# Performance work log

Measured on AMD Instinct MI355X. Metric: run time of the kernel, lower is better.

Reference implementation:

```python
import jax, jax.numpy as jnp
import numpy as np

NUM_HEADS = 8

def setup_inputs() -> dict:
    key = jax.random.key(0)
    ks = jax.random.split(key, 6)
    B, S, D, K = 2, 2048, 512, 64
    x = jax.random.normal(ks[0], (B, S, D), dtype=jnp.float32)
    routes = jax.random.randint(ks[1], (S, K), 0, S, dtype=jnp.int32)
    distances = jax.random.uniform(ks[2], (S, S), dtype=jnp.float32)
    W_in = jax.random.normal(ks[3], (D, D), dtype=jnp.float32) * (1.0 / np.sqrt(D))
    W_out = jax.random.normal(ks[4], (D, D), dtype=jnp.float32) * (1.0 / np.sqrt(D))
    b_out = jnp.zeros((D,), dtype=jnp.float32)
    return {"x": x, "routes": routes, "distances": distances,
            "W_in": W_in, "W_out": W_out, "b_out": b_out}

def reference(x, routes, distances, W_in, W_out, b_out):
    # x: [B,S,D]; routes: [S,K] int gather table; distances: [S,S]
    B, S, D = x.shape
    H = NUM_HEADS
    hd = D // H
    K = routes.shape[1]
    # in_proj (torch Linear, no bias): y = x @ W^T
    h = jnp.einsum('bsd,ed->bse', x, W_in).reshape(B, S, H, hd)
    # gather fusion windows via precomputed routes: [B,S,K,H,hd]
    gathered = h[:, routes]
    # weighted fusion: weights from precomputed Cantor distance matrix
    d = jnp.take_along_axis(distances, routes.astype(jnp.int32), axis=1)  # [S,K]
    w = jax.nn.softmax(-d, axis=-1)  # normalized fusion weights
    fused = jnp.einsum('sk,bskhd->bshd', w, gathered)  # [B,S,H,hd]
    fused = fused.reshape(B, S, D)
    # out_proj + residual (dropout is identity in eval)
    out = jnp.einsum('bsd,ed->bse', fused, W_out) + b_out
    return out + x
```

## Files before the change

### kernel.cpp

```cpp
#include <hip/hip_runtime.h>
#include <hip/hip_bf16.h>

#define S_DIM 2048
#define D_DIM 512
#define B_DIM 2
#define K_RT  64

typedef __attribute__((ext_vector_type(8))) short short8;
typedef __attribute__((ext_vector_type(4))) float f32x4;

static __device__ __forceinline__ float bf16lo_to_f(unsigned u) {
    union { unsigned u; float f; } c; c.u = u << 16; return c.f;
}
static __device__ __forceinline__ float bf16hi_to_f(unsigned u) {
    union { unsigned u; float f; } c; c.u = u & 0xffff0000u; return c.f;
}
static __device__ __forceinline__ unsigned short f_to_bf16(float f) {
    union { float f; unsigned u; } c; c.f = f;
    unsigned u = c.u;
    u += 0x7fffu + ((u >> 16) & 1u);
    return (unsigned short)(u >> 16);
}
static __device__ __forceinline__ unsigned pk2(float a, float b) {
    return (unsigned)f_to_bf16(a) | ((unsigned)f_to_bf16(b) << 16);
}

#define GBM 64
#define GBN 64
#define GBK 32
#define LROW 40

template<bool AF32, bool BF32, bool OUTF32>
__global__ __launch_bounds__(256) void gemm_bt(
    const void* __restrict__ Av, const void* __restrict__ Bv, void* __restrict__ Cv,
    const float* __restrict__ bias, const float* __restrict__ residual,
    int M, int N, int K)
{
    __shared__ unsigned short As[GBM * LROW];
    __shared__ unsigned short Bs[GBN * LROW];

    const int tid  = threadIdx.x;
    const int lane = tid & 63;
    const int wv   = tid >> 6;
    const int wm   = (wv & 1) * 32;
    const int wn   = (wv >> 1) * 32;
    const int m0   = blockIdx.y * GBM;
    const int n0   = blockIdx.x * GBN;

    const int lr = tid >> 2;
    const int lc = (tid & 3) * 8;

    const int mi = lane & 15;
    const int kg = lane >> 4;

    f32x4 acc[2][2] = {};

    for (int k0 = 0; k0 < K; k0 += GBK) {
        uint4 apk, bpk;
        if (AF32) {
            const float* A = (const float*)Av;
            const float4 a0 = *(const float4*)(A + (size_t)(m0 + lr) * K + k0 + lc);
            const float4 a1 = *(const float4*)(A + (size_t)(m0 + lr) * K + k0 + lc + 4);
            apk.x = pk2(a0.x, a0.y); apk.y = pk2(a0.z, a0.w);
            apk.z = pk2(a1.x, a1.y); apk.w = pk2(a1.z, a1.w);
        } else {
            const unsigned short* A = (const unsigned short*)Av;
            apk = *(const uint4*)(A + (size_t)(m0 + lr) * K + k0 + lc);
        }
        if (BF32) {
            const float* B = (const float*)Bv;
            const float4 b0 = *(const float4*)(B + (size_t)(n0 + lr) * K + k0 + lc);
            const float4 b1 = *(const float4*)(B + (size_t)(n0 + lr) * K + k0 + lc + 4);
            bpk.x = pk2(b0.x, b0.y); bpk.y = pk2(b0.z, b0.w);
            bpk.z = pk2(b1.x, b1.y); bpk.w = pk2(b1.z, b1.w);
        } else {
            const unsigned short* B = (const unsigned short*)Bv;
            bpk = *(const uint4*)(B + (size_t)(n0 + lr) * K + k0 + lc);
        }
        *(uint4*)(As + lr * LROW + lc) = apk;
        *(uint4*)(Bs + lr * LROW + lc) = bpk;
        __syncthreads();

        short8 af0 = *(const short8*)(As + (wm +      mi) * LROW + kg * 8);
        short8 af1 = *(const short8*)(As + (wm + 16 + mi) * LROW + kg * 8);
        short8 bf0 = *(const short8*)(Bs + (wn +      mi) * LROW + kg * 8);
        short8 bf1 = *(const short8*)(Bs + (wn + 16 + mi) * LROW + kg * 8);

        acc[0][0] = __builtin_amdgcn_mfma_f32_16x16x32_bf16(af0, bf0, acc[0][0], 0, 0, 0);
        acc[0][1] = __builtin_amdgcn_mfma_f32_16x16x32_bf16(af0, bf1, acc[0][1], 0, 0, 0);
        acc[1][0] = __builtin_amdgcn_mfma_f32_16x16x32_bf16(af1, bf0, acc[1][0], 0, 0, 0);
        acc[1][1] = __builtin_amdgcn_mfma_f32_16x16x32_bf16(af1, bf1, acc[1][1], 0, 0, 0);
        __syncthreads();
    }

    const int rb  = (lane >> 4) * 4;
    const int col = lane & 15;
    #pragma unroll
    for (int i = 0; i < 2; ++i) {
        #pragma unroll
        for (int j = 0; j < 2; ++j) {
            #pragma unroll
            for (int r = 0; r < 4; ++r) {
                const int m = m0 + wm + i * 16 + rb + r;
                const int n = n0 + wn + j * 16 + col;
                const float v = acc[i][j][r];
                if (OUTF32) {
                    ((float*)Cv)[(size_t)m * N + n] = v + bias[n] + residual[(size_t)m * N + n];
                } else {
                    ((unsigned short*)Cv)[(size_t)m * N + n] = f_to_bf16(v);
                }
            }
        }
    }
}

__global__ __launch_bounds__(256) void fuse_gather(
    const unsigned short* __restrict__ h, const int* __restrict__ routes,
    const float* __restrict__ distances, unsigned short* __restrict__ fused)
{
    const int tid  = threadIdx.x;
    const int lane = tid & 63;
    const int wv   = tid >> 6;
    const int s    = blockIdx.x * 4 + wv;
    const int b    = blockIdx.y;

    const int rt = routes[s * K_RT + lane];
    const float v = -distances[(size_t)s * S_DIM + rt];
    float mx = v;
    #pragma unroll
    for (int off = 32; off >= 1; off >>= 1) mx = fmaxf(mx, __shfl_xor(mx, off, 64));
    const float e = __expf(v - mx);
    float sum = e;
    #pragma unroll
    for (int off = 32; off >= 1; off >>= 1) sum += __shfl_xor(sum, off, 64);
    const float wl = e / sum;

    const unsigned short* hb = h + (size_t)b * S_DIM * D_DIM;
    float acc[8] = {};
    #pragma unroll 4
    for (int k = 0; k < 64; ++k) {
        const int   rk = __shfl(rt, k, 64);
        const float wk = __shfl(wl, k, 64);
        const uint4 p = *(const uint4*)(hb + (size_t)rk * D_DIM + lane * 8);
        acc[0] = fmaf(wk, bf16lo_to_f(p.x), acc[0]);
        acc[1] = fmaf(wk, bf16hi_to_f(p.x), acc[1]);
        acc[2] = fmaf(wk, bf16lo_to_f(p.y), acc[2]);
        acc[3] = fmaf(wk, bf16hi_to_f(p.y), acc[3]);
        acc[4] = fmaf(wk, bf16lo_to_f(p.z), acc[4]);
        acc[5] = fmaf(wk, bf16hi_to_f(p.z), acc[5]);
        acc[6] = fmaf(wk, bf16lo_to_f(p.w), acc[6]);
        acc[7] = fmaf(wk, bf16hi_to_f(p.w), acc[7]);
    }
    uint4 o;
    o.x = pk2(acc[0], acc[1]);
    o.y = pk2(acc[2], acc[3]);
    o.z = pk2(acc[4], acc[5]);
    o.w = pk2(acc[6], acc[7]);
    *(uint4*)(fused + ((size_t)b * S_DIM + s) * D_DIM + lane * 8) = o;
}

extern "C" void kernel_launch(void* const* d_in, const int* in_sizes, int n_in,
                              void* d_out, int out_size, void* d_ws, size_t ws_size,
                              hipStream_t stream) {
    const float* x         = (const float*)d_in[0];
    const int*   routes    = (const int*)  d_in[1];
    const float* distances = (const float*)d_in[2];
    const float* W_in      = (const float*)d_in[3];
    const float* W_out     = (const float*)d_in[4];
    const float* b_out     = (const float*)d_in[5];
    float* out = (float*)d_out;

    const int M = B_DIM * S_DIM;

    unsigned short* hb = (unsigned short*)d_ws;
    unsigned short* fb = hb + (size_t)M * D_DIM;

    const dim3 ggrid(D_DIM / GBN, M / GBM);

    gemm_bt<true, true, false><<<ggrid, 256, 0, stream>>>(
        x, W_in, hb, nullptr, nullptr, M, D_DIM, D_DIM);
    fuse_gather<<<dim3(S_DIM / 4, B_DIM), 256, 0, stream>>>(hb, routes, distances, fb);
    gemm_bt<false, true, true><<<ggrid, 256, 0, stream>>>(
        fb, W_out, out, b_out, x, M, D_DIM, D_DIM);
}
```

Measured before the change: 124.5 us.

## Merge GEMM, gather, and GEMM into one cooperative kernel with grid syncs

Replaces the three separate launches (in-proj GEMM, gather-fuse, out-proj GEMM) with one cooperative kernel of 512 blocks. Each block computes one 64x64 GEMM tile, waits at a grid-wide barrier, does 8 gather units, waits at another barrier, then computes the out-proj tile. This is meant to remove inter-kernel launch gaps. In exchange it adds grid-sync cost and caps the grid at a size that must be co-resident, which limits occupancy and latency hiding.

```diff
diff --git a/kernel.cpp b/kernel.cpp
--- a/kernel.cpp
+++ b/kernel.cpp
@@ -1,10 +1,14 @@
 #include <hip/hip_runtime.h>
 #include <hip/hip_bf16.h>
+#include <hip/hip_cooperative_groups.h>
+
+namespace cg = cooperative_groups;
 
 #define S_DIM 2048
 #define D_DIM 512
 #define B_DIM 2
 #define K_RT  64
+#define M_DIM 4096
 
 typedef __attribute__((ext_vector_type(8))) short short8;
 typedef __attribute__((ext_vector_type(4))) float f32x4;
@@ -30,22 +34,22 @@
 #define GBK 32
 #define LROW 40
 
-template<bool AF32, bool BF32, bool OUTF32>
-__global__ __launch_bounds__(256) void gemm_bt(
-    const void* __restrict__ Av, const void* __restrict__ Bv, void* __restrict__ Cv,
-    const float* __restrict__ bias, const float* __restrict__ residual,
-    int M, int N, int K)
+struct SMem {
+    unsigned short As[GBM * LROW];
+    unsigned short Bs[GBN * LROW];
+};
+
+template<bool AF32, bool OUTF32>
+static __device__ __forceinline__ void gemm_tile(
+    const void* __restrict__ Av, const float* __restrict__ Bw,
+    void* __restrict__ Cv, const float* __restrict__ bias,
+    const float* __restrict__ residual, SMem& sm, int m0, int n0)
 {
-    __shared__ unsigned short As[GBM * LROW];
-    __shared__ unsigned short Bs[GBN * LROW];
-
     const int tid  = threadIdx.x;
     const int lane = tid & 63;
     const int wv   = tid >> 6;
     const int wm   = (wv & 1) * 32;
     const int wn   = (wv >> 1) * 32;
-    const int m0   = blockIdx.y * GBM;
-    const int n0   = blockIdx.x * GBN;
 
     const int lr = tid >> 2;
     const int lc = (tid & 3) * 8;
@@ -55,36 +59,32 @@
 
     f32x4 acc[2][2] = {};
 
-    for (int k0 = 0; k0 < K; k0 += GBK) {
+    for (int k0 = 0; k0 < D_DIM; k0 += GBK) {
         uint4 apk, bpk;
         if (AF32) {
             const float* A = (const float*)Av;
-            const float4 a0 = *(const float4*)(A + (size_t)(m0 + lr) * K + k0 + lc);
-            const float4 a1 = *(const float4*)(A + (size_t)(m0 + lr) * K + k0 + lc + 4);
+            const float4 a0 = *(const float4*)(A + (size_t)(m0 + lr) * D_DIM + k0 + lc);
+            const float4 a1 = *(const float4*)(A + (size_t)(m0 + lr) * D_DIM + k0 + lc + 4);
             apk.x = pk2(a0.x, a0.y); apk.y = pk2(a0.z, a0.w);
             apk.z = pk2(a1.x, a1.y); apk.w = pk2(a1.z, a1.w);
         } else {
             const unsigned short* A = (const unsigned short*)Av;
-            apk = *(const uint4*)(A + (size_t)(m0 + lr) * K + k0 + lc);
-        }
-        if (BF32) {
-            const float* B = (const float*)Bv;
-            const float4 b0 = *(const float4*)(B + (size_t)(n0 + lr) * K + k0 + lc);
-            const float4 b1 = *(const float4*)(B + (size_t)(n0 + lr) * K + k0 + lc + 4);
+            apk = *(const uint4*)(A + (size_t)(m0 + lr) * D_DIM + k0 + lc);
+        }
+        {
+            const float4 b0 = *(const float4*)(Bw + (size_t)(n0 + lr) * D_DIM + k0 + lc);
+            const float4 b1 = *(const float4*)(Bw + (size_t)(n0 + lr) * D_DIM + k0 + lc + 4);
             bpk.x = pk2(b0.x, b0.y); bpk.y = pk2(b0.z, b0.w);
             bpk.z = pk2(b1.x, b1.y); bpk.w = pk2(b1.z, b1.w);
-        } else {
-            const unsigned short* B = (const unsigned short*)Bv;
-            bpk = *(const uint4*)(B + (size_t)(n0 + lr) * K + k0 + lc);
-        }
-        *(uint4*)(As + lr * LROW + lc) = apk;
-        *(uint4*)(Bs + lr * LROW + lc) = bpk;
+        }
+        *(uint4*)(sm.As + lr * LROW + lc) = apk;
+        *(uint4*)(sm.Bs + lr * LROW + lc) = bpk;
         __syncthreads();
 
-        short8 af0 = *(const short8*)(As + (wm +      mi) * LROW + kg * 8);
-        short8 af1 = *(const short8*)(As + (wm + 16 + mi) * LROW + kg * 8);
-        short8 bf0 = *(const short8*)(Bs + (wn +      mi) * LROW + kg * 8);
-        short8 bf1 = *(const short8*)(Bs + (wn + 16 + mi) * LROW + kg * 8);
+        short8 af0 = *(const short8*)(sm.As + (wm +      mi) * LROW + kg * 8);
+        short8 af1 = *(const short8*)(sm.As + (wm + 16 + mi) * LROW + kg * 8);
+        short8 bf0 = *(const short8*)(sm.Bs + (wn +      mi) * LROW + kg * 8);
+        short8 bf1 = *(const short8*)(sm.Bs + (wn + 16 + mi) * LROW + kg * 8);
 
         acc[0][0] = __builtin_amdgcn_mfma_f32_16x16x32_bf16(af0, bf0, acc[0][0], 0, 0, 0);
         acc[0][1] = __builtin_amdgcn_mfma_f32_16x16x32_bf16(af0, bf1, acc[0][1], 0, 0, 0);
@@ -105,25 +105,20 @@
                 const int n = n0 + wn + j * 16 + col;
                 const float v = acc[i][j][r];
                 if (OUTF32) {
-                    ((float*)Cv)[(size_t)m * N + n] = v + bias[n] + residual[(size_t)m * N + n];
+                    ((float*)Cv)[(size_t)m * D_DIM + n] = v + bias[n] + residual[(size_t)m * D_DIM + n];
                 } else {
-                    ((unsigned short*)Cv)[(size_t)m * N + n] = f_to_bf16(v);
+                    ((unsigned short*)Cv)[(size_t)m * D_DIM + n] = f_to_bf16(v);
                 }
             }
         }
     }
 }
 
-__global__ __launch_bounds__(256) void fuse_gather(
+static __device__ __forceinline__ void fuse_unit(
     const unsigned short* __restrict__ h, const int* __restrict__ routes,
-    const float* __restrict__ distances, unsigned short* __restrict__ fused)
+    const float* __restrict__ distances, unsigned short* __restrict__ fused,
+    int b, int s, int lane)
 {
-    const int tid  = threadIdx.x;
-    const int lane = tid & 63;
-    const int wv   = tid >> 6;
-    const int s    = blockIdx.x * 4 + wv;
-    const int b    = blockIdx.y;
-
     const int rt = routes[s * K_RT + lane];
     const float v = -distances[(size_t)s * S_DIM + rt];
     float mx = v;
@@ -159,6 +154,35 @@
     *(uint4*)(fused + ((size_t)b * S_DIM + s) * D_DIM + lane * 8) = o;
 }
 
+__global__ __launch_bounds__(256, 2) void mega(
+    const float* __restrict__ x, const int* __restrict__ routes,
+    const float* __restrict__ distances, const float* __restrict__ W_in,
+    const float* __restrict__ W_out, const float* __restrict__ b_out,
+    float* __restrict__ out, unsigned short* __restrict__ hb,
+    unsigned short* __restrict__ fb)
+{
+    __shared__ SMem sm;
+    const int bx = blockIdx.x;
+    const int m0 = (bx >> 3) * GBM;
+    const int n0 = (bx & 7) * GBN;
+
+    gemm_tile<true, false>(x, W_in, hb, nullptr, nullptr, sm, m0, n0);
+    cg::this_grid().sync();
+
+    {
+        const int lane = threadIdx.x & 63;
+        const int wv   = threadIdx.x >> 6;
+        #pragma unroll
+        for (int i = 0; i < 2; ++i) {
+            const int unit = bx * 8 + wv * 2 + i;
+            fuse_unit(hb, routes, distances, fb, unit >> 11, unit & (S_DIM - 1), lane);
+        }
+    }
+    cg::this_grid().sync();
+
+    gemm_tile<false, true>(fb, W_out, out, b_out, x, sm, m0, n0);
+}
+
 extern "C" void kernel_launch(void* const* d_in, const int* in_sizes, int n_in,
                               void* d_out, int out_size, void* d_ws, size_t ws_size,
                               hipStream_t stream) {
@@ -170,16 +194,12 @@
     const float* b_out     = (const float*)d_in[5];
     float* out = (float*)d_out;
 
-    const int M = B_DIM * S_DIM;
-
     unsigned short* hb = (unsigned short*)d_ws;
-    unsigned short* fb = hb + (size_t)M * D_DIM;
-
-    const dim3 ggrid(D_DIM / GBN, M / GBM);
-
-    gemm_bt<true, true, false><<<ggrid, 256, 0, stream>>>(
-        x, W_in, hb, nullptr, nullptr, M, D_DIM, D_DIM);
-    fuse_gather<<<dim3(S_DIM / 4, B_DIM), 256, 0, stream>>>(hb, routes, distances, fb);
-    gemm_bt<false, true, true><<<ggrid, 256, 0, stream>>>(
-        fb, W_out, out, b_out, x, M, D_DIM, D_DIM);
-}
+    unsigned short* fb = hb + (size_t)M_DIM * D_DIM;
+
+    void* args[] = {
+        (void*)&x, (void*)&routes, (void*)&distances, (void*)&W_in,
+        (void*)&W_out, (void*)&b_out, (void*)&out, (void*)&hb, (void*)&fb
+    };
+    hipLaunchCooperativeKernel((const void*)mega, dim3(512), dim3(256), args, 0, stream);
+}
```

New measurement: 250.2 us. +100.9%, slower.
